# Kernel optimization log

Hardware: AMD Instinct MI355X
Metric: run time of the kernel (lower is better)

Reference implementation:

```python
import jax, jax.numpy as jnp
import numpy as np
from jax.scipy.special import logsumexp

NUM_STATES = 16
NUM_CHAINS = 8
NUM_NODES = 1500
NUM_ITERS = 500


def setup_inputs() -> dict:
    key = jax.random.key(0)
    k1, k2, k3, k4 = jax.random.split(key, 4)
    return {
        "unnormalized_state_init": jax.random.normal(k1, (NUM_STATES, NUM_CHAINS), jnp.float32),
        "unnormalized_chain_weights": jax.random.normal(k2, (NUM_ITERS, NUM_CHAINS), jnp.float32),
        "unnormalized_emission_matrix": jax.random.normal(k3, (NUM_STATES, 1, NUM_NODES), jnp.float32),
        "unnormalized_transition_matrix": jax.random.normal(k4, (NUM_CHAINS, NUM_STATES, NUM_STATES), jnp.float32),
    }


def reference(unnormalized_state_init, unnormalized_chain_weights,
              unnormalized_emission_matrix, unnormalized_transition_matrix):
    # log_transform_params: normalize each distribution in log domain
    log_state_init = jax.nn.log_softmax(unnormalized_state_init, axis=0)          # (S,C): over states
    log_chain_weights = jax.nn.log_softmax(unnormalized_chain_weights, axis=-1)   # (T,C): over chains
    log_emission = jax.nn.log_softmax(unnormalized_emission_matrix, axis=-1)      # (S,1,N): over nodes
    log_T_ = jax.nn.log_softmax(unnormalized_transition_matrix, axis=-1)          # (C,S,S): over next state

    T = unnormalized_chain_weights.shape[0]

    # chain-marginalized transition matrix (computed as in torch forward_model; not used downstream)
    log_mean_cw = logsumexp(log_chain_weights, axis=0) - jnp.log(jnp.asarray(T, log_chain_weights.dtype))
    _log_transition_matrix = logsumexp(log_T_ + log_mean_cw[:, None, None], axis=0)

    # sequential HMM prior recursion over tiny (S,C) state via scan
    def step(h, _):
        # h: (S,C) -> h.T: (C,S); logsumexp over previous-state axis
        new = logsumexp(h.T[:, :, None] + log_T_, axis=1).T  # (S,C)
        return new, new

    h0 = log_state_init
    _, hs = jax.lax.scan(step, h0, None, length=T - 1)
    log_hidden_state_probs = jnp.concatenate([h0[None], hs], axis=0)  # (T,S,C)

    # emission broadcast: (S,1,N) + (T,S,C,1) -> (T,S,C,N), then add chain weights
    log_observed_state_probs_ = (log_emission[None]
                                 + log_hidden_state_probs[..., None]
                                 + log_chain_weights[:, None, :, None])
    # marginalize over states then chains
    log_observed_state_probs = logsumexp(log_observed_state_probs_, axis=(1, 2))  # (T,N)
    return (log_observed_state_probs, log_observed_state_probs_, log_hidden_state_probs)
```

## Files before the change

### kernel.cpp

```cpp
#include <hip/hip_runtime.h>
#include <hip/hip_bf16.h>

#define S 16
#define C 8
#define SC 128
#define TT 500
#define NN 1500
#define NF4 375
#define CHUNK 25
#define NCHUNK 20

__device__ __forceinline__ float fexp2(float x) { return exp2f(x); }
__device__ __forceinline__ float flog2(float x) { return log2f(x); }

#define L2E 1.4426950408889634f
#define LN2 0.6931471805599453f

typedef float f4v __attribute__((ext_vector_type(4)));

#define MM(dst, Asrc, Bsrc) do {                                          \
    __syncthreads();                                                      \
    {   const int c_ = tid >> 5; const int e0_ = tid & 31;                \
        for (int r_ = 0; r_ < 8; ++r_) {                                  \
            const int e_ = e0_ + (r_ << 5);                               \
            const int i_ = e_ >> 4; const int l_ = e_ & 15;               \
            float acc_ = 0.f;                                             \
            _Pragma("unroll")                                             \
            for (int s_ = 0; s_ < S; ++s_)                                \
                acc_ += Asrc[(c_ * S + i_) * S + s_] *                    \
                        Bsrc[(c_ * S + s_) * S + l_];                     \
            dst[(c_ * S + i_) * S + l_] = acc_;                          \
        } }                                                               \
} while (0)

__global__ __launch_bounds__(256) void hmm_setup(
    const float* __restrict__ usi,
    const float* __restrict__ ucw,
    const float* __restrict__ uem,
    const float* __restrict__ utm,
    float* __restrict__ ws_lcw,
    float* __restrict__ ws_cwp,
    float* __restrict__ ws_pT,
    float* __restrict__ ws_q,
    float* __restrict__ ws_emlse)
{
    __shared__ float bufT[C * S * S];
    __shared__ float bufX[C * S * S];
    __shared__ float bufY[C * S * S];
    __shared__ float bufZ[C * S * S];
    __shared__ float qbuf[C * S];
    const int tid = threadIdx.x;

    for (int t = tid; t < TT; t += 256) {
        float x[C]; float m = -1e30f;
#pragma unroll
        for (int cc = 0; cc < C; ++cc) { x[cc] = ucw[t * C + cc]; m = fmaxf(m, x[cc]); }
        float acc = 0.f;
#pragma unroll
        for (int cc = 0; cc < C; ++cc) acc += fexp2((x[cc] - m) * L2E);
        const float lse = m + flog2(acc) * LN2;
#pragma unroll
        for (int cc = 0; cc < C; ++cc) {
            const float v = x[cc] - lse;
            ws_lcw[t * C + cc] = v;
            ws_cwp[t * C + cc] = fexp2(v * L2E);
        }
    }

    {
        const int row = tid >> 4;
        const int ln  = tid & 15;
        const float* rp = uem + row * NN;
        float a = 0.f;
        for (int n = ln; n < NN; n += 16) a += fexp2(rp[n] * L2E);
#pragma unroll
        for (int off = 8; off >= 1; off >>= 1) a += __shfl_xor(a, off);
        if (ln == 0) ws_emlse[row] = flog2(a) * LN2;
    }

    if (tid < SC) {
        float x[S]; float m = -1e30f;
#pragma unroll
        for (int k = 0; k < S; ++k) { x[k] = utm[tid * S + k]; m = fmaxf(m, x[k]); }
        float acc = 0.f; float e[S];
#pragma unroll
        for (int k = 0; k < S; ++k) { e[k] = fexp2((x[k] - m) * L2E); acc += e[k]; }
        const float inv = 1.f / acc;
#pragma unroll
        for (int k = 0; k < S; ++k) {
            const float v = e[k] * inv;
            bufT[tid * S + k] = v;
            ws_pT[tid * S + k] = v;
        }
    }

    if (tid < C) {
        const int cc = tid;
        float x[S]; float m = -1e30f;
#pragma unroll
        for (int s0 = 0; s0 < S; ++s0) { x[s0] = usi[s0 * C + cc]; m = fmaxf(m, x[s0]); }
        float acc = 0.f; float e[S];
#pragma unroll
        for (int s0 = 0; s0 < S; ++s0) { e[s0] = fexp2((x[s0] - m) * L2E); acc += e[s0]; }
        const float inv = 1.f / acc;
#pragma unroll
        for (int s0 = 0; s0 < S; ++s0) {
            const float v = e[s0] * inv;
            qbuf[cc * S + s0] = v;
            ws_q[cc * S + s0] = v;
        }
    }

    MM(bufX, bufT, bufT);
    MM(bufY, bufX, bufX);
    MM(bufZ, bufY, bufY);
    MM(bufX, bufZ, bufZ);
    MM(bufY, bufX, bufZ);
    MM(bufX, bufY, bufT);
    __syncthreads();

    const int c5 = tid >> 4;
    const int l5 = tid & 15;
    float Acol[S];
    if (tid < 128) {
#pragma unroll
        for (int s0 = 0; s0 < S; ++s0) Acol[s0] = bufX[(c5 * S + s0) * S + l5];
    }
    for (int k = 1; k < NCHUNK; ++k) {
        float acc = 0.f;
        if (tid < 128) {
#pragma unroll
            for (int s0 = 0; s0 < S; ++s0) acc += qbuf[c5 * S + s0] * Acol[s0];
        }
        __syncthreads();
        if (tid < 128) {
            qbuf[c5 * S + l5] = acc;
            ws_q[k * SC + c5 * S + l5] = acc;
        }
        __syncthreads();
    }
}

__global__ __launch_bounds__(64) void hmm_chunks(
    const float* __restrict__ ws_pT,
    const float* __restrict__ ws_q,
    const float* __restrict__ ws_cwp,
    const float* __restrict__ ws_emlse,
    float* __restrict__ out3,
    float* __restrict__ ws_gval)
{
    const int k = blockIdx.x;
    const int lane = threadIdx.x;
    const int c = lane >> 3;
    const int j = lane & 7;

    float Ta[S], Tb[S];
#pragma unroll
    for (int s0 = 0; s0 < S; ++s0) {
        Ta[s0] = ws_pT[(c * S + s0) * S + j];
        Tb[s0] = ws_pT[(c * S + s0) * S + j + 8];
    }
    float pa = ws_q[k * SC + c * S + j];
    float pb = ws_q[k * SC + c * S + j + 8];
    const float invEa = fexp2(-ws_emlse[j] * L2E);
    const float invEb = fexp2(-ws_emlse[j + 8] * L2E);

    const int base = c << 3;
    for (int i = 0; i < CHUNK; ++i) {
        const int t = k * CHUNK + i;
        const float la = flog2(pa) * LN2;
        const float lb = flog2(pb) * LN2;
        out3[(size_t)t * SC + j * C + c]       = la;
        out3[(size_t)t * SC + (j + 8) * C + c] = lb;

        const float cw = ws_cwp[t * C + c];
        float ea = pa * cw, eb = pb * cw;
        ea += __shfl_xor(ea, 8); ea += __shfl_xor(ea, 16); ea += __shfl_xor(ea, 32);
        eb += __shfl_xor(eb, 8); eb += __shfl_xor(eb, 16); eb += __shfl_xor(eb, 32);
        if (lane < 8) {
            ws_gval[t * S + lane]     = ea * invEa;
            ws_gval[t * S + lane + 8] = eb * invEb;
        }
        if (i == CHUNK - 1) break;

        float pv[S];
#pragma unroll
        for (int q = 0; q < 8; ++q) {
            pv[q]     = __shfl(pa, base + q);
            pv[q + 8] = __shfl(pb, base + q);
        }
        float a0 = 0.f, a1 = 0.f, a2 = 0.f, a3 = 0.f;
        float b0 = 0.f, b1 = 0.f, b2 = 0.f, b3 = 0.f;
#pragma unroll
        for (int s0 = 0; s0 < S; s0 += 4) {
            a0 = fmaf(pv[s0],     Ta[s0],     a0);
            a1 = fmaf(pv[s0 + 1], Ta[s0 + 1], a1);
            a2 = fmaf(pv[s0 + 2], Ta[s0 + 2], a2);
            a3 = fmaf(pv[s0 + 3], Ta[s0 + 3], a3);
            b0 = fmaf(pv[s0],     Tb[s0],     b0);
            b1 = fmaf(pv[s0 + 1], Tb[s0 + 1], b1);
            b2 = fmaf(pv[s0 + 2], Tb[s0 + 2], b2);
            b3 = fmaf(pv[s0 + 3], Tb[s0 + 3], b3);
        }
        pa = (a0 + a1) + (a2 + a3);
        pb = (b0 + b1) + (b2 + b3);
    }
}

__global__ __launch_bounds__(256) void stream_kernel(
    const float* __restrict__ uem,
    const float* __restrict__ out3,
    const float* __restrict__ ws_lcw,
    const float* __restrict__ ws_emlse,
    float* __restrict__ out2)
{
    const int tid = threadIdx.x;
    const int row0 = blockIdx.x << 5;
    float* outp = out2 + (size_t)row0 * NN;

    for (int rr = 0; rr < 16; ++rr) {
        const int r0 = row0 + rr * 2;
        const int t  = r0 >> 7;
        const int s  = (r0 >> 3) & 15;
        const int c0 = r0 & 7;
        const float el = ws_emlse[s];
        const float av0 = out3[r0]     + ws_lcw[t * C + c0]     - el;
        const float av1 = out3[r0 + 1] + ws_lcw[t * C + c0 + 1] - el;
        const float* rowp = uem + s * NN;
        float* po = outp + (size_t)rr * 2 * NN;
#pragma unroll
        for (int off = tid; off < 750; off += 256) {
            const bool hi = off >= NF4;
            const float a = hi ? av1 : av0;
            const int o = hi ? off - NF4 : off;
            f4v e = *(const f4v*)(rowp + o * 4);
            e += a;
            *(f4v*)(po + (size_t)off * 4) = e;
        }
    }
}

__global__ __launch_bounds__(256) void out1_kernel(
    const float* __restrict__ uem,
    const float* __restrict__ ws_gval,
    float* __restrict__ out1)
{
    const int t = blockIdx.x;
    const int tid = threadIdx.x;
    __shared__ float g[S];
    if (tid < S) g[tid] = ws_gval[t * S + tid];
    __syncthreads();

    for (int idx = tid; idx < NF4; idx += 256) {
        f4v acc = {0.f, 0.f, 0.f, 0.f};
#pragma unroll
        for (int s0 = 0; s0 < S; ++s0) {
            const f4v e = *(const f4v*)(uem + s0 * NN + idx * 4);
            const float gs = g[s0];
            acc.x += fexp2(e.x * L2E) * gs;
            acc.y += fexp2(e.y * L2E) * gs;
            acc.z += fexp2(e.z * L2E) * gs;
            acc.w += fexp2(e.w * L2E) * gs;
        }
        f4v r;
        r.x = flog2(acc.x) * LN2;
        r.y = flog2(acc.y) * LN2;
        r.z = flog2(acc.z) * LN2;
        r.w = flog2(acc.w) * LN2;
        *(f4v*)(out1 + (size_t)t * NN + idx * 4) = r;
    }
}

extern "C" void kernel_launch(void* const* d_in, const int* in_sizes, int n_in,
                              void* d_out, int out_size, void* d_ws, size_t ws_size,
                              hipStream_t stream)
{
    const float* usi = (const float*)d_in[0];
    const float* ucw = (const float*)d_in[1];
    const float* uem = (const float*)d_in[2];
    const float* utm = (const float*)d_in[3];

    float* out  = (float*)d_out;
    float* out1 = out;
    float* out2 = out + 750000;
    float* out3 = out + 750000 + 96000000;

    float* ws       = (float*)d_ws;
    float* ws_lcw   = ws;
    float* ws_cwp   = ws + 4000;
    float* ws_pT    = ws + 8000;
    float* ws_q     = ws + 10048;
    float* ws_emlse = ws + 12608;
    float* ws_gval  = ws + 12624;

    hmm_setup<<<1, 256, 0, stream>>>(usi, ucw, uem, utm,
                                     ws_lcw, ws_cwp, ws_pT, ws_q, ws_emlse);
    hmm_chunks<<<NCHUNK, 64, 0, stream>>>(ws_pT, ws_q, ws_cwp, ws_emlse,
                                          out3, ws_gval);
    stream_kernel<<<2000, 256, 0, stream>>>(uem, out3, ws_lcw, ws_emlse, out2);
    out1_kernel<<<TT, 256, 0, stream>>>(uem, ws_gval, out1);
}
```

Baseline: 132.2 us.

## Fuse all stages into one cooperative persistent kernel with grid syncs

Replaces the four separate launches with a single cooperative kernel of 768 blocks. Setup work is split across three blocks, then chunked recursion runs on 16 blocks, then out1 and the large out2 broadcast stream run across all blocks, with grid.sync between phases. Chunk size changes to 32 with 16 chunks, and the per-row add values are precomputed into a workspace array. The aim is to remove launch gaps and serial setup latency, at the cost of grid-wide barriers and a static per-block split of the dominant 384MB write.

```diff
diff --git a/kernel.cpp b/kernel.cpp
--- a/kernel.cpp
+++ b/kernel.cpp
@@ -1,14 +1,21 @@
 #include <hip/hip_runtime.h>
+#include <hip/hip_cooperative_groups.h>
 #include <hip/hip_bf16.h>
+
+namespace cg = cooperative_groups;
 
 #define S 16
 #define C 8
 #define SC 128
 #define TT 500
 #define NN 1500
-#define NF4 375
-#define CHUNK 25
-#define NCHUNK 20
+#define NR4 375
+#define CHUNK 32
+#define NCHUNK 16
+#define NB 768
+#define TPB 256
+#define FCH 31250
+#define TOTF4 24000000
 
 __device__ __forceinline__ float fexp2(float x) { return exp2f(x); }
 __device__ __forceinline__ float flog2(float x) { return log2f(x); }
@@ -33,41 +40,109 @@
         } }                                                               \
 } while (0)
 
-__global__ __launch_bounds__(256) void hmm_setup(
+__global__ __launch_bounds__(TPB, 4) void mono(
     const float* __restrict__ usi,
     const float* __restrict__ ucw,
     const float* __restrict__ uem,
     const float* __restrict__ utm,
+    float* __restrict__ out1,
+    float* __restrict__ out2,
+    float* __restrict__ out3,
     float* __restrict__ ws_lcw,
     float* __restrict__ ws_cwp,
     float* __restrict__ ws_pT,
     float* __restrict__ ws_q,
-    float* __restrict__ ws_emlse)
+    float* __restrict__ ws_emlse,
+    float* __restrict__ ws_gval,
+    float* __restrict__ ws_addv)
 {
-    __shared__ float bufT[C * S * S];
-    __shared__ float bufX[C * S * S];
-    __shared__ float bufY[C * S * S];
-    __shared__ float bufZ[C * S * S];
-    __shared__ float qbuf[C * S];
+    __shared__ float B0[C * S * S];
+    __shared__ float B1[C * S * S];
+    __shared__ float B2[C * S * S];
+    __shared__ float qbuf[SC];
+    __shared__ float cwS[CHUNK * C];
+    __shared__ float lcwS[CHUNK * C];
+    __shared__ float emS[S];
+
+    const int bid = blockIdx.x;
     const int tid = threadIdx.x;
-
-    for (int t = tid; t < TT; t += 256) {
-        float x[C]; float m = -1e30f;
-#pragma unroll
-        for (int cc = 0; cc < C; ++cc) { x[cc] = ucw[t * C + cc]; m = fmaxf(m, x[cc]); }
-        float acc = 0.f;
-#pragma unroll
-        for (int cc = 0; cc < C; ++cc) acc += fexp2((x[cc] - m) * L2E);
-        const float lse = m + flog2(acc) * LN2;
-#pragma unroll
-        for (int cc = 0; cc < C; ++cc) {
-            const float v = x[cc] - lse;
-            ws_lcw[t * C + cc] = v;
-            ws_cwp[t * C + cc] = fexp2(v * L2E);
-        }
-    }
-
-    {
+    cg::grid_group grid = cg::this_grid();
+
+    if (bid == 0) {
+        if (tid < SC) {
+            float x[S]; float m = -1e30f;
+#pragma unroll
+            for (int k = 0; k < S; ++k) { x[k] = utm[tid * S + k]; m = fmaxf(m, x[k]); }
+            float acc = 0.f; float e[S];
+#pragma unroll
+            for (int k = 0; k < S; ++k) { e[k] = fexp2((x[k] - m) * L2E); acc += e[k]; }
+            const float inv = 1.f / acc;
+#pragma unroll
+            for (int k = 0; k < S; ++k) {
+                const float v = e[k] * inv;
+                B0[tid * S + k] = v;
+                ws_pT[tid * S + k] = v;
+            }
+        }
+        if (tid < C) {
+            const int cc = tid;
+            float x[S]; float m = -1e30f;
+#pragma unroll
+            for (int s0 = 0; s0 < S; ++s0) { x[s0] = usi[s0 * C + cc]; m = fmaxf(m, x[s0]); }
+            float acc = 0.f; float e[S];
+#pragma unroll
+            for (int s0 = 0; s0 < S; ++s0) { e[s0] = fexp2((x[s0] - m) * L2E); acc += e[s0]; }
+            const float inv = 1.f / acc;
+#pragma unroll
+            for (int s0 = 0; s0 < S; ++s0) {
+                const float v = e[s0] * inv;
+                qbuf[cc * S + s0] = v;
+                ws_q[cc * S + s0] = v;
+            }
+        }
+        MM(B1, B0, B0);
+        MM(B2, B1, B1);
+        MM(B1, B2, B2);
+        MM(B2, B1, B1);
+        MM(B1, B2, B2);
+        __syncthreads();
+        const int c5 = tid >> 4;
+        const int l5 = tid & 15;
+        float Acol[S];
+        if (tid < SC) {
+#pragma unroll
+            for (int s0 = 0; s0 < S; ++s0) Acol[s0] = B1[(c5 * S + s0) * S + l5];
+        }
+        for (int k = 1; k < NCHUNK; ++k) {
+            float acc = 0.f;
+            if (tid < SC) {
+#pragma unroll
+                for (int s0 = 0; s0 < S; ++s0) acc += qbuf[c5 * S + s0] * Acol[s0];
+            }
+            __syncthreads();
+            if (tid < SC) {
+                qbuf[c5 * S + l5] = acc;
+                ws_q[k * SC + c5 * S + l5] = acc;
+            }
+            __syncthreads();
+        }
+    } else if (bid == 1) {
+        for (int t = tid; t < TT; t += TPB) {
+            float x[C]; float m = -1e30f;
+#pragma unroll
+            for (int cc = 0; cc < C; ++cc) { x[cc] = ucw[t * C + cc]; m = fmaxf(m, x[cc]); }
+            float acc = 0.f;
+#pragma unroll
+            for (int cc = 0; cc < C; ++cc) acc += fexp2((x[cc] - m) * L2E);
+            const float lse = m + flog2(acc) * LN2;
+#pragma unroll
+            for (int cc = 0; cc < C; ++cc) {
+                const float v = x[cc] - lse;
+                ws_lcw[t * C + cc] = v;
+                ws_cwp[t * C + cc] = fexp2(v * L2E);
+            }
+        }
+    } else if (bid == 2) {
         const int row = tid >> 4;
         const int ln  = tid & 15;
         const float* rp = uem + row * NN;
@@ -77,197 +152,123 @@
         for (int off = 8; off >= 1; off >>= 1) a += __shfl_xor(a, off);
         if (ln == 0) ws_emlse[row] = flog2(a) * LN2;
     }
-
-    if (tid < SC) {
-        float x[S]; float m = -1e30f;
-#pragma unroll
-        for (int k = 0; k < S; ++k) { x[k] = utm[tid * S + k]; m = fmaxf(m, x[k]); }
-        float acc = 0.f; float e[S];
-#pragma unroll
-        for (int k = 0; k < S; ++k) { e[k] = fexp2((x[k] - m) * L2E); acc += e[k]; }
-        const float inv = 1.f / acc;
-#pragma unroll
-        for (int k = 0; k < S; ++k) {
-            const float v = e[k] * inv;
-            bufT[tid * S + k] = v;
-            ws_pT[tid * S + k] = v;
+    __threadfence();
+    grid.sync();
+
+    if (bid < NCHUNK) {
+        const int k = bid;
+        {
+            const int t = k * CHUNK + (tid >> 3);
+            if (t < TT) {
+                cwS[tid]  = ws_cwp[t * C + (tid & 7)];
+                lcwS[tid] = ws_lcw[t * C + (tid & 7)];
+            }
+        }
+        if (tid < S) emS[tid] = ws_emlse[tid];
+        __syncthreads();
+        if (tid < 64) {
+            const int c = tid >> 3;
+            const int j = tid & 7;
+            float Ta[S], Tb[S];
+#pragma unroll
+            for (int s0 = 0; s0 < S; ++s0) {
+                Ta[s0] = ws_pT[(c * S + s0) * S + j];
+                Tb[s0] = ws_pT[(c * S + s0) * S + j + 8];
+            }
+            float pa = ws_q[k * SC + c * S + j];
+            float pb = ws_q[k * SC + c * S + j + 8];
+            const float ela = emS[j];
+            const float elb = emS[j + 8];
+            const float invEa = fexp2(-ela * L2E);
+            const float invEb = fexp2(-elb * L2E);
+            const int base = c << 3;
+
+            for (int i = 0; i < CHUNK; ++i) {
+                const int t = k * CHUNK + i;
+                if (t >= TT) break;
+                const float la = flog2(pa) * LN2;
+                const float lb = flog2(pb) * LN2;
+                out3[(size_t)t * SC + j * C + c]       = la;
+                out3[(size_t)t * SC + (j + 8) * C + c] = lb;
+                const float w = lcwS[i * C + c];
+                ws_addv[t * SC + j * C + c]       = la + w - ela;
+                ws_addv[t * SC + (j + 8) * C + c] = lb + w - elb;
+
+                const float cw = cwS[i * C + c];
+                float ea = pa * cw, eb = pb * cw;
+                ea += __shfl_xor(ea, 8); ea += __shfl_xor(ea, 16); ea += __shfl_xor(ea, 32);
+                eb += __shfl_xor(eb, 8); eb += __shfl_xor(eb, 16); eb += __shfl_xor(eb, 32);
+                if (tid < 8) {
+                    ws_gval[t * S + j]     = ea * invEa;
+                    ws_gval[t * S + j + 8] = eb * invEb;
+                }
+                if (i < CHUNK - 1) {
+                    float pv[S];
+#pragma unroll
+                    for (int q = 0; q < 8; ++q) {
+                        pv[q]     = __shfl(pa, base + q);
+                        pv[q + 8] = __shfl(pb, base + q);
+                    }
+                    float a0 = 0.f, a1 = 0.f, a2 = 0.f, a3 = 0.f;
+                    float b0 = 0.f, b1 = 0.f, b2 = 0.f, b3 = 0.f;
+#pragma unroll
+                    for (int s0 = 0; s0 < S; s0 += 4) {
+                        a0 = fmaf(pv[s0],     Ta[s0],     a0);
+                        a1 = fmaf(pv[s0 + 1], Ta[s0 + 1], a1);
+                        a2 = fmaf(pv[s0 + 2], Ta[s0 + 2], a2);
+                        a3 = fmaf(pv[s0 + 3], Ta[s0 + 3], a3);
+                        b0 = fmaf(pv[s0],     Tb[s0],     b0);
+                        b1 = fmaf(pv[s0 + 1], Tb[s0 + 1], b1);
+                        b2 = fmaf(pv[s0 + 2], Tb[s0 + 2], b2);
+                        b3 = fmaf(pv[s0 + 3], Tb[s0 + 3], b3);
+                    }
+                    pa = (a0 + a1) + (a2 + a3);
+                    pb = (b0 + b1) + (b2 + b3);
+                }
+            }
         }
     }
-
-    if (tid < C) {
-        const int cc = tid;
-        float x[S]; float m = -1e30f;
-#pragma unroll
-        for (int s0 = 0; s0 < S; ++s0) { x[s0] = usi[s0 * C + cc]; m = fmaxf(m, x[s0]); }
-        float acc = 0.f; float e[S];
-#pragma unroll
-        for (int s0 = 0; s0 < S; ++s0) { e[s0] = fexp2((x[s0] - m) * L2E); acc += e[s0]; }
-        const float inv = 1.f / acc;
-#pragma unroll
-        for (int s0 = 0; s0 < S; ++s0) {
-            const float v = e[s0] * inv;
-            qbuf[cc * S + s0] = v;
-            ws_q[cc * S + s0] = v;
+    __threadfence();
+    grid.sync();
+
+    {
+        const int f = bid * TPB + tid;
+        if (f < TT * NR4) {
+            const unsigned t = (unsigned)f / NR4;
+            const int n4 = f - (int)t * NR4;
+            const f4v* uem4 = (const f4v*)uem;
+            const float* gv = ws_gval + t * S;
+            f4v acc = {0.f, 0.f, 0.f, 0.f};
+#pragma unroll
+            for (int s0 = 0; s0 < S; ++s0) {
+                const f4v e = uem4[s0 * NR4 + n4];
+                const float g = gv[s0];
+                acc.x += fexp2(e.x * L2E) * g;
+                acc.y += fexp2(e.y * L2E) * g;
+                acc.z += fexp2(e.z * L2E) * g;
+                acc.w += fexp2(e.w * L2E) * g;
+            }
+            f4v r;
+            r.x = flog2(acc.x) * LN2;
+            r.y = flog2(acc.y) * LN2;
+            r.z = flog2(acc.z) * LN2;
+            r.w = flog2(acc.w) * LN2;
+            ((f4v*)out1)[f] = r;
         }
     }
-
-    MM(bufX, bufT, bufT);
-    MM(bufY, bufX, bufX);
-    MM(bufZ, bufY, bufY);
-    MM(bufX, bufZ, bufZ);
-    MM(bufY, bufX, bufZ);
-    MM(bufX, bufY, bufT);
-    __syncthreads();
-
-    const int c5 = tid >> 4;
-    const int l5 = tid & 15;
-    float Acol[S];
-    if (tid < 128) {
-#pragma unroll
-        for (int s0 = 0; s0 < S; ++s0) Acol[s0] = bufX[(c5 * S + s0) * S + l5];
-    }
-    for (int k = 1; k < NCHUNK; ++k) {
-        float acc = 0.f;
-        if (tid < 128) {
-#pragma unroll
-            for (int s0 = 0; s0 < S; ++s0) acc += qbuf[c5 * S + s0] * Acol[s0];
-        }
-        __syncthreads();
-        if (tid < 128) {
-            qbuf[c5 * S + l5] = acc;
-            ws_q[k * SC + c5 * S + l5] = acc;
-        }
-        __syncthreads();
-    }
-}
-
-__global__ __launch_bounds__(64) void hmm_chunks(
-    const float* __restrict__ ws_pT,
-    const float* __restrict__ ws_q,
-    const float* __restrict__ ws_cwp,
-    const float* __restrict__ ws_emlse,
-    float* __restrict__ out3,
-    float* __restrict__ ws_gval)
-{
-    const int k = blockIdx.x;
-    const int lane = threadIdx.x;
-    const int c = lane >> 3;
-    const int j = lane & 7;
-
-    float Ta[S], Tb[S];
-#pragma unroll
-    for (int s0 = 0; s0 < S; ++s0) {
-        Ta[s0] = ws_pT[(c * S + s0) * S + j];
-        Tb[s0] = ws_pT[(c * S + s0) * S + j + 8];
-    }
-    float pa = ws_q[k * SC + c * S + j];
-    float pb = ws_q[k * SC + c * S + j + 8];
-    const float invEa = fexp2(-ws_emlse[j] * L2E);
-    const float invEb = fexp2(-ws_emlse[j + 8] * L2E);
-
-    const int base = c << 3;
-    for (int i = 0; i < CHUNK; ++i) {
-        const int t = k * CHUNK + i;
-        const float la = flog2(pa) * LN2;
-        const float lb = flog2(pb) * LN2;
-        out3[(size_t)t * SC + j * C + c]       = la;
-        out3[(size_t)t * SC + (j + 8) * C + c] = lb;
-
-        const float cw = ws_cwp[t * C + c];
-        float ea = pa * cw, eb = pb * cw;
-        ea += __shfl_xor(ea, 8); ea += __shfl_xor(ea, 16); ea += __shfl_xor(ea, 32);
-        eb += __shfl_xor(eb, 8); eb += __shfl_xor(eb, 16); eb += __shfl_xor(eb, 32);
-        if (lane < 8) {
-            ws_gval[t * S + lane]     = ea * invEa;
-            ws_gval[t * S + lane + 8] = eb * invEb;
-        }
-        if (i == CHUNK - 1) break;
-
-        float pv[S];
-#pragma unroll
-        for (int q = 0; q < 8; ++q) {
-            pv[q]     = __shfl(pa, base + q);
-            pv[q + 8] = __shfl(pb, base + q);
-        }
-        float a0 = 0.f, a1 = 0.f, a2 = 0.f, a3 = 0.f;
-        float b0 = 0.f, b1 = 0.f, b2 = 0.f, b3 = 0.f;
-#pragma unroll
-        for (int s0 = 0; s0 < S; s0 += 4) {
-            a0 = fmaf(pv[s0],     Ta[s0],     a0);
-            a1 = fmaf(pv[s0 + 1], Ta[s0 + 1], a1);
-            a2 = fmaf(pv[s0 + 2], Ta[s0 + 2], a2);
-            a3 = fmaf(pv[s0 + 3], Ta[s0 + 3], a3);
-            b0 = fmaf(pv[s0],     Tb[s0],     b0);
-            b1 = fmaf(pv[s0 + 1], Tb[s0 + 1], b1);
-            b2 = fmaf(pv[s0 + 2], Tb[s0 + 2], b2);
-            b3 = fmaf(pv[s0 + 3], Tb[s0 + 3], b3);
-        }
-        pa = (a0 + a1) + (a2 + a3);
-        pb = (b0 + b1) + (b2 + b3);
-    }
-}
-
-__global__ __launch_bounds__(256) void stream_kernel(
-    const float* __restrict__ uem,
-    const float* __restrict__ out3,
-    const float* __restrict__ ws_lcw,
-    const float* __restrict__ ws_emlse,
-    float* __restrict__ out2)
-{
-    const int tid = threadIdx.x;
-    const int row0 = blockIdx.x << 5;
-    float* outp = out2 + (size_t)row0 * NN;
-
-    for (int rr = 0; rr < 16; ++rr) {
-        const int r0 = row0 + rr * 2;
-        const int t  = r0 >> 7;
-        const int s  = (r0 >> 3) & 15;
-        const int c0 = r0 & 7;
-        const float el = ws_emlse[s];
-        const float av0 = out3[r0]     + ws_lcw[t * C + c0]     - el;
-        const float av1 = out3[r0 + 1] + ws_lcw[t * C + c0 + 1] - el;
-        const float* rowp = uem + s * NN;
-        float* po = outp + (size_t)rr * 2 * NN;
-#pragma unroll
-        for (int off = tid; off < 750; off += 256) {
-            const bool hi = off >= NF4;
-            const float a = hi ? av1 : av0;
-            const int o = hi ? off - NF4 : off;
-            f4v e = *(const f4v*)(rowp + o * 4);
-            e += a;
-            *(f4v*)(po + (size_t)off * 4) = e;
-        }
-    }
-}
-
-__global__ __launch_bounds__(256) void out1_kernel(
-    const float* __restrict__ uem,
-    const float* __restrict__ ws_gval,
-    float* __restrict__ out1)
-{
-    const int t = blockIdx.x;
-    const int tid = threadIdx.x;
-    __shared__ float g[S];
-    if (tid < S) g[tid] = ws_gval[t * S + tid];
-    __syncthreads();
-
-    for (int idx = tid; idx < NF4; idx += 256) {
-        f4v acc = {0.f, 0.f, 0.f, 0.f};
-#pragma unroll
-        for (int s0 = 0; s0 < S; ++s0) {
-            const f4v e = *(const f4v*)(uem + s0 * NN + idx * 4);
-            const float gs = g[s0];
-            acc.x += fexp2(e.x * L2E) * gs;
-            acc.y += fexp2(e.y * L2E) * gs;
-            acc.z += fexp2(e.z * L2E) * gs;
-            acc.w += fexp2(e.w * L2E) * gs;
-        }
-        f4v r;
-        r.x = flog2(acc.x) * LN2;
-        r.y = flog2(acc.y) * LN2;
-        r.z = flog2(acc.z) * LN2;
-        r.w = flog2(acc.w) * LN2;
-        *(f4v*)(out1 + (size_t)t * NN + idx * 4) = r;
+    {
+        const f4v* uem4 = (const f4v*)uem;
+        f4v* o2 = (f4v*)out2;
+        const int f0 = bid * FCH;
+        const int f1 = (f0 + FCH < TOTF4) ? f0 + FCH : TOTF4;
+        for (int f = f0 + tid; f < f1; f += TPB) {
+            const unsigned r = (unsigned)f / NR4;
+            const int n4 = f - (int)r * NR4;
+            const int s = ((int)r >> 3) & 15;
+            f4v e = uem4[s * NR4 + n4];
+            e += ws_addv[r];
+            o2[f] = e;
+        }
     }
 }
 
@@ -290,13 +291,15 @@
     float* ws_cwp   = ws + 4000;
     float* ws_pT    = ws + 8000;
     float* ws_q     = ws + 10048;
-    float* ws_emlse = ws + 12608;
-    float* ws_gval  = ws + 12624;
-
-    hmm_setup<<<1, 256, 0, stream>>>(usi, ucw, uem, utm,
-                                     ws_lcw, ws_cwp, ws_pT, ws_q, ws_emlse);
-    hmm_chunks<<<NCHUNK, 64, 0, stream>>>(ws_pT, ws_q, ws_cwp, ws_emlse,
-                                          out3, ws_gval);
-    stream_kernel<<<2000, 256, 0, stream>>>(uem, out3, ws_lcw, ws_emlse, out2);
-    out1_kernel<<<TT, 256, 0, stream>>>(uem, ws_gval, out1);
+    float* ws_emlse = ws + 12096;
+    float* ws_gval  = ws + 12112;
+    float* ws_addv  = ws + 20112;
+
+    void* args[] = {
+        (void*)&usi, (void*)&ucw, (void*)&uem, (void*)&utm,
+        (void*)&out1, (void*)&out2, (void*)&out3,
+        (void*)&ws_lcw, (void*)&ws_cwp, (void*)&ws_pT, (void*)&ws_q,
+        (void*)&ws_emlse, (void*)&ws_gval, (void*)&ws_addv
+    };
+    hipLaunchCooperativeKernel((void*)mono, dim3(NB), dim3(TPB), args, 0, stream);
 }
```

Result: slower. 362.8 us (+174.4%).
